# Optimization experiments

Hardware: AMD Instinct MI355X
Metric: run time of the kernel (lower is better)

The kernel has to match this reference:

```python
import jax, jax.numpy as jnp
import numpy as np

N_NODES = 100000
N_EDGES = 625000
D_IN = 128
D_OUT = 128


def setup_inputs() -> dict:
    key = jax.random.key(0)
    k1, k2, k3, k4 = jax.random.split(key, 4)
    embeds = jax.random.normal(k1, (N_NODES, D_IN), dtype=jnp.float32)
    weight = jax.random.normal(k2, (D_IN, D_OUT), dtype=jnp.float32)
    # COO sparse adjacency: row 0 = destination node, row 1 = source node
    edge_index = jax.random.randint(k3, (2, N_DGES := N_EDGES), 0, N_NODES, dtype=jnp.int32)
    edge_vals = jax.random.uniform(k4, (N_EDGES,), dtype=jnp.float32)
    return {"embeds": embeds, "weight": weight, "edge_index": edge_index, "edge_vals": edge_vals}


def reference(embeds, weight, edge_index, edge_vals):
    # support = embeds @ W  -> [N, D_OUT]
    support = jnp.matmul(embeds, weight)
    dst, src = edge_index[0], edge_index[1]
    # spmm: out[d] = sum_{e: dst[e]==d} vals[e] * support[src[e]]
    msgs = edge_vals[:, None] * support[src]  # [E, D_OUT]
    output = jax.ops.segment_sum(msgs, dst, num_segments=embeds.shape[0])
    return output
```

## Files before the change

### kernel.cpp

```cpp
#include <hip/hip_runtime.h>

#define D 128
#define CB 256
#define CB_SHIFT 8
#define NB_MAX 512

typedef __attribute__((ext_vector_type(8))) short short8;
typedef __attribute__((ext_vector_type(4))) float f32x4;

__device__ inline ushort f2bf(float f) {
    uint u = __float_as_uint(f);
    uint r = (u + 0x7FFFu + ((u >> 16) & 1u)) >> 16;
    return (ushort)r;
}

__device__ inline uint cvtpk(float lo, float hi) {
    uint r;
    asm("v_cvt_pk_bf16_f32 %0, %1, %2" : "=v"(r) : "v"(lo), "v"(hi));
    return r;
}


__global__ void zero_f4_kernel(float4* __restrict__ out, int n4) {
    int i = blockIdx.x * blockDim.x + threadIdx.x;
    int stride = gridDim.x * blockDim.x;
    float4 z = make_float4(0.f, 0.f, 0.f, 0.f);
    for (; i < n4; i += stride) out[i] = z;
}


__global__ __launch_bounds__(256) void bucket_hist(const int* __restrict__ dst,
                                                   int* __restrict__ bhist,
                                                   int* __restrict__ cbase,
                                                   int* __restrict__ ccursor, int E,
                                                   const float* __restrict__ W,
                                                   ushort* __restrict__ wT) {
    __shared__ int h[NB_MAX];
    __shared__ int scanbuf[256];
    __shared__ int lastFlag;
    const int t = threadIdx.x;
    #pragma unroll
    for (int j = t; j < NB_MAX; j += 256) h[j] = 0;

    const int gt = blockIdx.x * 256 + t;
    if (gt < D * D) { int r = gt >> 7, c = gt & 127; wT[c * D + r] = f2bf(W[gt]); }
    __syncthreads();

    const int stride = gridDim.x * 256;
    for (int i = gt; i < E; i += stride) atomicAdd(&h[dst[i] >> CB_SHIFT], 1);
    __syncthreads();
    #pragma unroll
    for (int j = t; j < NB_MAX; j += 256)
        if (h[j]) atomicAdd(&bhist[j], h[j]);

    __threadfence();
    __syncthreads();
    if (t == 0) lastFlag = (atomicAdd(&bhist[NB_MAX], 1) == (int)gridDim.x - 1);
    __syncthreads();
    if (!lastFlag) return;

    const int a = atomicAdd(&bhist[2 * t], 0);
    const int b = atomicAdd(&bhist[2 * t + 1], 0);
    const int s = a + b;
    scanbuf[t] = s;
    __syncthreads();
    for (int off = 1; off < 256; off <<= 1) {
        int x = (t >= off) ? scanbuf[t - off] : 0;
        __syncthreads();
        scanbuf[t] += x;
        __syncthreads();
    }
    const int excl = scanbuf[t] - s;
    cbase[2 * t] = excl;         ccursor[2 * t] = excl;
    cbase[2 * t + 1] = excl + a; ccursor[2 * t + 1] = excl + a;
    if (t == 255) cbase[NB_MAX] = excl + s;
}


__global__ __launch_bounds__(512) void gemm_part(const float* __restrict__ embeds,
                                                 const ushort* __restrict__ wT,
                                                 ushort* __restrict__ support, int N,
                                                 const int* __restrict__ dst,
                                                 const int* __restrict__ srcp,
                                                 const float* __restrict__ vals,
                                                 int* __restrict__ ccursor,
                                                 int2* __restrict__ pay1, int E, int npart) {
    __shared__ ushort bLds[D * D];
    __shared__ int phist[NB_MAX];
    __shared__ int pbase[NB_MAX];
    const int t = threadIdx.x;

    if ((int)blockIdx.x < npart) {
        const int ntile = (E + 2047) >> 11;
        for (int tile = blockIdx.x; tile < ntile; tile += npart) {
            const int e0 = tile << 11;
            if (t < NB_MAX) phist[t] = 0;
            __syncthreads();

            int bk[4], rk[4];
            #pragma unroll
            for (int j = 0; j < 4; ++j) {
                int e = e0 + j * 512 + t;
                bk[j] = -1;
                if (e < E) {
                    bk[j] = dst[e] >> CB_SHIFT;
                    rk[j] = atomicAdd(&phist[bk[j]], 1);
                }
            }
            __syncthreads();

            if (t < NB_MAX) pbase[t] = phist[t] ? atomicAdd(&ccursor[t], phist[t]) : 0;
            __syncthreads();

            #pragma unroll
            for (int j = 0; j < 4; ++j) {
                int e = e0 + j * 512 + t;
                if (e >= E) continue;
                int d = dst[e];
                int key = ((d & (CB - 1)) << 17) | srcp[e];
                pay1[pbase[bk[j]] + rk[j]] = make_int2(key, __float_as_int(vals[e]));
            }
            __syncthreads();
        }
        return;
    }

    const int gbid = blockIdx.x - npart;
    const int ngemm = gridDim.x - npart;
    const int w = t >> 6;
    const int l = t & 63;
    const int kgrp = l >> 4;
    const int lan15 = l & 15;

    #pragma unroll
    for (int c = 0; c < 4; ++c) {
        int chunk = c * 512 + t;
        int byteoff = chunk * 16;
        int n = byteoff >> 8;
        int dstoff = byteoff ^ ((n & 7) << 4);
        *(float4*)((char*)bLds + dstoff) = *(const float4*)((const char*)wT + byteoff);
    }
    __syncthreads();

    const int ntiles = (N + 127) >> 7;

    for (int tile = gbid; tile < ntiles; tile += ngemm) {
        const int row0 = tile << 7;
        const int grow = row0 + w * 16 + lan15;
        const bool valid = grow < N;
        const float* arow = embeds + (size_t)grow * D + kgrp * 8;

        float4 pf[8];
        if (valid) {
            #pragma unroll
            for (int ks = 0; ks < 4; ++ks) {
                pf[2 * ks]     = *(const float4*)(arow + ks * 32);
                pf[2 * ks + 1] = *(const float4*)(arow + ks * 32 + 4);
            }
        } else {
            #pragma unroll
            for (int j = 0; j < 8; ++j) pf[j] = make_float4(0.f, 0.f, 0.f, 0.f);
        }

        f32x4 acc[8];
        #pragma unroll
        for (int ct = 0; ct < 8; ++ct) acc[ct] = (f32x4)0.0f;

        #pragma unroll
        for (int ks = 0; ks < 4; ++ks) {
            union { uint4 u; short8 s; } cv;
            const float4 f0 = pf[2 * ks], f1 = pf[2 * ks + 1];
            cv.u.x = cvtpk(f0.x, f0.y);
            cv.u.y = cvtpk(f0.z, f0.w);
            cv.u.z = cvtpk(f1.x, f1.y);
            cv.u.w = cvtpk(f1.z, f1.w);
            const short8 af = cv.s;

            const int kbyte = ks * 64 + kgrp * 16;
            #pragma unroll
            for (int ct = 0; ct < 8; ++ct) {
                const int n = ct * 16 + lan15;
                const int boff = (n * 256 + kbyte) ^ ((n & 7) << 4);
                short8 bfr = *(const short8*)((const char*)bLds + boff);
                acc[ct] = __builtin_amdgcn_mfma_f32_16x16x32_bf16(af, bfr, acc[ct], 0, 0, 0);
            }
        }

        #pragma unroll
        for (int r = 0; r < 4; ++r) {
            const int orow = row0 + w * 16 + kgrp * 4 + r;
            if (orow < N) {
                ushort* srow = &support[(size_t)orow * D + lan15];
                #pragma unroll
                for (int cp = 0; cp < 4; ++cp) {
                    uint u = cvtpk(acc[2 * cp][r], acc[2 * cp + 1][r]);
                    srow[(2 * cp) * 16] = (ushort)u;
                    srow[(2 * cp + 1) * 16] = (ushort)(u >> 16);
                }
            }
        }
    }
}


__global__ __launch_bounds__(256) void finefill2(const int2* __restrict__ pay1,
                                                 const int* __restrict__ cbase,
                                                 int* __restrict__ offsets,
                                                 int2* __restrict__ pay,
                                                 int N, int nb, int E) {
    __shared__ int lcnt[CB];
    __shared__ int bs[CB];
    __shared__ int lofs[CB];
    const int t = threadIdx.x;

    for (int b = blockIdx.x; b < nb; b += gridDim.x) {
        const int beg = cbase[b];
        const int end = cbase[b + 1];
        const int d0 = b << CB_SHIFT;

        lcnt[t] = 0;
        __syncthreads();
        for (int i = beg + t; i < end; i += 256)
            atomicAdd(&lcnt[((unsigned)pay1[i].x) >> 17], 1);
        __syncthreads();

        const int c = lcnt[t];
        bs[t] = c;
        __syncthreads();
        for (int off = 1; off < 256; off <<= 1) {
            int x = (t >= off) ? bs[t - off] : 0;
            __syncthreads();
            bs[t] += x;
            __syncthreads();
        }
        const int run = bs[t] - c + beg;
        if (d0 + t < N) offsets[d0 + t] = run;
        lofs[t] = run;
        __syncthreads();

        for (int i = beg + t; i < end; i += 256) {
            int2 p = pay1[i];
            int dl = ((unsigned)p.x) >> 17;
            int pos = atomicAdd(&lofs[dl], 1);
            pay[pos] = make_int2(p.x & 0x1FFFF, p.y);
        }
        __syncthreads();
    }
    if (blockIdx.x == 0 && t == 0) offsets[N] = E;
}


#define EDGE_MAC(P, M)                                          \
    do {                                                        \
        const float v_ = __int_as_float((P).y);                 \
        acc[0] += v_ * __uint_as_float(((M).x & 0xFFFFu) << 16);\
        acc[1] += v_ * __uint_as_float((M).x & 0xFFFF0000u);    \
        acc[2] += v_ * __uint_as_float(((M).y & 0xFFFFu) << 16);\
        acc[3] += v_ * __uint_as_float((M).y & 0xFFFF0000u);    \
        acc[4] += v_ * __uint_as_float(((M).z & 0xFFFFu) << 16);\
        acc[5] += v_ * __uint_as_float((M).z & 0xFFFF0000u);    \
        acc[6] += v_ * __uint_as_float(((M).w & 0xFFFFu) << 16);\
        acc[7] += v_ * __uint_as_float((M).w & 0xFFFF0000u);    \
    } while (0)

__global__ __launch_bounds__(256, 8) void gather_kernel(const ushort* __restrict__ support,
                                                        const int* __restrict__ offsets,
                                                        const int2* __restrict__ pay,
                                                        float* __restrict__ out, int N) {
    const int gid = (blockIdx.x * 256 + threadIdx.x) >> 4;
    const int sl = threadIdx.x & 15;
    if (gid >= N) return;

    const int beg = offsets[gid];
    const int end = offsets[gid + 1];

    float acc[8];
    #pragma unroll
    for (int j = 0; j < 8; ++j) acc[j] = 0.f;

    int i = beg;
    for (; i + 3 < end; i += 4) {
        const int2 p0 = pay[i], p1 = pay[i + 1], p2 = pay[i + 2], p3 = pay[i + 3];
        const uint4 m0 = *(const uint4*)&support[(size_t)p0.x * D + sl * 8];
        const uint4 m1 = *(const uint4*)&support[(size_t)p1.x * D + sl * 8];
        const uint4 m2 = *(const uint4*)&support[(size_t)p2.x * D + sl * 8];
        const uint4 m3 = *(const uint4*)&support[(size_t)p3.x * D + sl * 8];
        EDGE_MAC(p0, m0); EDGE_MAC(p1, m1); EDGE_MAC(p2, m2); EDGE_MAC(p3, m3);
    }
    for (; i + 1 < end; i += 2) {
        const int2 p0 = pay[i], p1 = pay[i + 1];
        const uint4 m0 = *(const uint4*)&support[(size_t)p0.x * D + sl * 8];
        const uint4 m1 = *(const uint4*)&support[(size_t)p1.x * D + sl * 8];
        EDGE_MAC(p0, m0); EDGE_MAC(p1, m1);
    }
    if (i < end) {
        const int2 p0 = pay[i];
        const uint4 m0 = *(const uint4*)&support[(size_t)p0.x * D + sl * 8];
        EDGE_MAC(p0, m0);
    }

    float* o = &out[(size_t)gid * D + sl * 8];
    *(float4*)o       = make_float4(acc[0], acc[1], acc[2], acc[3]);
    *(float4*)(o + 4) = make_float4(acc[4], acc[5], acc[6], acc[7]);
}


__global__ __launch_bounds__(256) void scatter_kernel(const ushort* __restrict__ support,
                                                      const int* __restrict__ dst,
                                                      const int* __restrict__ src,
                                                      const float* __restrict__ vals,
                                                      float* __restrict__ out, int E) {
    const long long tid = (long long)blockIdx.x * blockDim.x + threadIdx.x;
    const int e = (int)(tid >> 6);
    if (e >= E) return;
    const int c = ((int)tid & 63) * 2;

    const int s = src[e];
    const int d = dst[e];
    const float v = vals[e];

    const uint m = *(const uint*)&support[(size_t)s * D + c];
    const float mx = __uint_as_float((m & 0xFFFFu) << 16);
    const float my = __uint_as_float(m & 0xFFFF0000u);
    atomicAdd(&out[(size_t)d * D + c + 0], v * mx);
    atomicAdd(&out[(size_t)d * D + c + 1], v * my);
}


static inline char* align256(char* p) {
    return (char*)(((uintptr_t)p + 255) & ~(uintptr_t)255);
}

extern "C" void kernel_launch(void* const* d_in, const int* in_sizes, int n_in,
                              void* d_out, int out_size, void* d_ws, size_t ws_size,
                              hipStream_t stream) {
    const float* embeds = (const float*)d_in[0];
    const float* W      = (const float*)d_in[1];
    const int*   eidx   = (const int*)d_in[2];
    const float* vals   = (const float*)d_in[3];

    const int N = in_sizes[0] / D;
    const int E = in_sizes[3];
    const int* dstp = eidx;
    const int* srcp = eidx + E;

    float* out = (float*)d_out;

    char* p = (char*)d_ws;
    ushort* support = (ushort*)p;  p = align256(p + (size_t)N * D * 2);
    ushort* wT      = (ushort*)p;  p = align256(p + (size_t)D * D * 2);
    int* offsets    = (int*)p;     p = align256(p + (size_t)(N + 1) * 4);
    int* bhist      = (int*)p;     p = align256(p + (NB_MAX + 1) * 4);
    int* cbase      = (int*)p;     p = align256(p + (NB_MAX + 1) * 4);
    int* ccursor    = (int*)p;     p = align256(p + NB_MAX * 4);
    int2* pay       = (int2*)p;    p = align256(p + (size_t)E * 8);
    int2* pay1      = (int2*)p;    p = align256(p + (size_t)E * 8);
    const size_t needed = (size_t)(p - (char*)d_ws);

    const int nb = (N + CB - 1) / CB;
    const bool two_level = (N <= (1 << 17)) && (nb <= NB_MAX) && (ws_size >= needed);

    if (two_level) {
        hipMemsetAsync(bhist, 0, (NB_MAX + 1) * 4, stream);
        bucket_hist<<<128, 256, 0, stream>>>(dstp, bhist, cbase, ccursor, E, W, wT);

        const int ntile = (E + 2047) / 2048;
        const int npart = ntile < 512 ? ntile : 512;
        gemm_part<<<npart + 512, 512, 0, stream>>>(embeds, wT, support, N,
                                                   dstp, srcp, vals, ccursor, pay1, E, npart);

        finefill2<<<nb, 256, 0, stream>>>(pay1, cbase, offsets, pay, N, nb, E);
        gather_kernel<<<(N * 16 + 255) / 256, 256, 0, stream>>>(support, offsets, pay, out, N);
    } else {
        hipMemsetAsync(bhist, 0, (NB_MAX + 1) * 4, stream);
        bucket_hist<<<128, 256, 0, stream>>>(dstp, bhist, cbase, ccursor, E, W, wT);
        gemm_part<<<512, 512, 0, stream>>>(embeds, wT, support, N,
                                           dstp, srcp, vals, ccursor, pay1, E, 0);
        zero_f4_kernel<<<2048, 256, 0, stream>>>((float4*)out, out_size / 4);
        const long long nthreads = (long long)E * 64;
        const int blocks = (int)((nthreads + 255) / 256);
        scatter_kernel<<<blocks, 256, 0, stream>>>(support, dstp, srcp, vals, out, E);
    }
}
```

Measured before the change: 92.80 us.

## Split GEMM tiles across partition and fine-fill kernels to overlap work

The dense GEMM now runs in two parts. The first 60% of row tiles are computed alongside the edge partition pass, and the rest run alongside the fine bucket fill in a new fused gemm_fill kernel. The fine fill moves to 512-thread blocks with one bucket per block. The aim is to balance load so the memory-bound fill work overlaps MFMA work instead of running as a separate, underused launch. The bucket_hist grid size is also doubled. This adds a fixed 3/5 split ratio that may not suit other shapes, and gemm_fill blocks carry a large LDS footprint even when they only do fill work.

```diff
diff --git a/kernel.cpp b/kernel.cpp
--- a/kernel.cpp
+++ b/kernel.cpp
@@ -18,6 +18,85 @@
     uint r;
     asm("v_cvt_pk_bf16_f32 %0, %1, %2" : "=v"(r) : "v"(lo), "v"(hi));
     return r;
+}
+
+
+__device__ __forceinline__ void gemm_run(const float* __restrict__ embeds,
+                                         const ushort* __restrict__ wT,
+                                         ushort* __restrict__ support, int N,
+                                         ushort* bLds, int t,
+                                         int tile0, int tileEnd, int stride) {
+    const int w = t >> 6;
+    const int l = t & 63;
+    const int kgrp = l >> 4;
+    const int lan15 = l & 15;
+
+    #pragma unroll
+    for (int c = 0; c < 4; ++c) {
+        int chunk = c * 512 + t;
+        int byteoff = chunk * 16;
+        int n = byteoff >> 8;
+        int dstoff = byteoff ^ ((n & 7) << 4);
+        *(float4*)((char*)bLds + dstoff) = *(const float4*)((const char*)wT + byteoff);
+    }
+    __syncthreads();
+
+    for (int tile = tile0; tile < tileEnd; tile += stride) {
+        const int row0 = tile << 7;
+        const int grow = row0 + w * 16 + lan15;
+        const bool valid = grow < N;
+        const float* arow = embeds + (size_t)grow * D + kgrp * 8;
+
+        float4 pf[8];
+        if (valid) {
+            #pragma unroll
+            for (int ks = 0; ks < 4; ++ks) {
+                pf[2 * ks]     = *(const float4*)(arow + ks * 32);
+                pf[2 * ks + 1] = *(const float4*)(arow + ks * 32 + 4);
+            }
+        } else {
+            #pragma unroll
+            for (int j = 0; j < 8; ++j) pf[j] = make_float4(0.f, 0.f, 0.f, 0.f);
+        }
+
+        f32x4 acc[8];
+        #pragma unroll
+        for (int ct = 0; ct < 8; ++ct) acc[ct] = (f32x4)0.0f;
+
+        #pragma unroll
+        for (int ks = 0; ks < 4; ++ks) {
+            union { uint4 u; short8 s; } cv;
+            const float4 f0 = pf[2 * ks], f1 = pf[2 * ks + 1];
+            cv.u.x = cvtpk(f0.x, f0.y);
+            cv.u.y = cvtpk(f0.z, f0.w);
+            cv.u.z = cvtpk(f1.x, f1.y);
+            cv.u.w = cvtpk(f1.z, f1.w);
+            const short8 af = cv.s;
+
+            const int kbyte = ks * 64 + kgrp * 16;
+            #pragma unroll
+            for (int ct = 0; ct < 8; ++ct) {
+                const int n = ct * 16 + lan15;
+                const int boff = (n * 256 + kbyte) ^ ((n & 7) << 4);
+                short8 bfr = *(const short8*)((const char*)bLds + boff);
+                acc[ct] = __builtin_amdgcn_mfma_f32_16x16x32_bf16(af, bfr, acc[ct], 0, 0, 0);
+            }
+        }
+
+        #pragma unroll
+        for (int r = 0; r < 4; ++r) {
+            const int orow = row0 + w * 16 + kgrp * 4 + r;
+            if (orow < N) {
+                ushort* srow = &support[(size_t)orow * D + lan15];
+                #pragma unroll
+                for (int cp = 0; cp < 4; ++cp) {
+                    uint u = cvtpk(acc[2 * cp][r], acc[2 * cp + 1][r]);
+                    srow[(2 * cp) * 16] = (ushort)u;
+                    srow[(2 * cp + 1) * 16] = (ushort)(u >> 16);
+                }
+            }
+        }
+    }
 }
 
 
@@ -84,7 +163,8 @@
                                                  const int* __restrict__ srcp,
                                                  const float* __restrict__ vals,
                                                  int* __restrict__ ccursor,
-                                                 int2* __restrict__ pay1, int E, int npart) {
+                                                 int2* __restrict__ pay1, int E,
+                                                 int npart, int T1) {
     __shared__ ushort bLds[D * D];
     __shared__ int phist[NB_MAX];
     __shared__ int pbase[NB_MAX];
@@ -125,128 +205,66 @@
         return;
     }
 
-    const int gbid = blockIdx.x - npart;
-    const int ngemm = gridDim.x - npart;
-    const int w = t >> 6;
-    const int l = t & 63;
-    const int kgrp = l >> 4;
-    const int lan15 = l & 15;
-
-    #pragma unroll
-    for (int c = 0; c < 4; ++c) {
-        int chunk = c * 512 + t;
-        int byteoff = chunk * 16;
-        int n = byteoff >> 8;
-        int dstoff = byteoff ^ ((n & 7) << 4);
-        *(float4*)((char*)bLds + dstoff) = *(const float4*)((const char*)wT + byteoff);
-    }
-    __syncthreads();
-
-    const int ntiles = (N + 127) >> 7;
-
-    for (int tile = gbid; tile < ntiles; tile += ngemm) {
-        const int row0 = tile << 7;
-        const int grow = row0 + w * 16 + lan15;
-        const bool valid = grow < N;
-        const float* arow = embeds + (size_t)grow * D + kgrp * 8;
-
-        float4 pf[8];
-        if (valid) {
-            #pragma unroll
-            for (int ks = 0; ks < 4; ++ks) {
-                pf[2 * ks]     = *(const float4*)(arow + ks * 32);
-                pf[2 * ks + 1] = *(const float4*)(arow + ks * 32 + 4);
-            }
-        } else {
-            #pragma unroll
-            for (int j = 0; j < 8; ++j) pf[j] = make_float4(0.f, 0.f, 0.f, 0.f);
-        }
-
-        f32x4 acc[8];
-        #pragma unroll
-        for (int ct = 0; ct < 8; ++ct) acc[ct] = (f32x4)0.0f;
-
-        #pragma unroll
-        for (int ks = 0; ks < 4; ++ks) {
-            union { uint4 u; short8 s; } cv;
-            const float4 f0 = pf[2 * ks], f1 = pf[2 * ks + 1];
-            cv.u.x = cvtpk(f0.x, f0.y);
-            cv.u.y = cvtpk(f0.z, f0.w);
-            cv.u.z = cvtpk(f1.x, f1.y);
-            cv.u.w = cvtpk(f1.z, f1.w);
-            const short8 af = cv.s;
-
-            const int kbyte = ks * 64 + kgrp * 16;
-            #pragma unroll
-            for (int ct = 0; ct < 8; ++ct) {
-                const int n = ct * 16 + lan15;
-                const int boff = (n * 256 + kbyte) ^ ((n & 7) << 4);
-                short8 bfr = *(const short8*)((const char*)bLds + boff);
-                acc[ct] = __builtin_amdgcn_mfma_f32_16x16x32_bf16(af, bfr, acc[ct], 0, 0, 0);
-            }
-        }
-
-        #pragma unroll
-        for (int r = 0; r < 4; ++r) {
-            const int orow = row0 + w * 16 + kgrp * 4 + r;
-            if (orow < N) {
-                ushort* srow = &support[(size_t)orow * D + lan15];
-                #pragma unroll
-                for (int cp = 0; cp < 4; ++cp) {
-                    uint u = cvtpk(acc[2 * cp][r], acc[2 * cp + 1][r]);
-                    srow[(2 * cp) * 16] = (ushort)u;
-                    srow[(2 * cp + 1) * 16] = (ushort)(u >> 16);
-                }
-            }
-        }
-    }
-}
-
-
-__global__ __launch_bounds__(256) void finefill2(const int2* __restrict__ pay1,
+    gemm_run(embeds, wT, support, N, bLds, t,
+             (int)blockIdx.x - npart, T1, (int)gridDim.x - npart);
+}
+
+
+__global__ __launch_bounds__(512) void gemm_fill(const float* __restrict__ embeds,
+                                                 const ushort* __restrict__ wT,
+                                                 ushort* __restrict__ support, int N,
+                                                 const int2* __restrict__ pay1,
                                                  const int* __restrict__ cbase,
                                                  int* __restrict__ offsets,
                                                  int2* __restrict__ pay,
-                                                 int N, int nb, int E) {
+                                                 int nb, int E, int T1) {
+    __shared__ ushort bLds[D * D];
     __shared__ int lcnt[CB];
-    __shared__ int bs[CB];
+    __shared__ int sbuf[512];
     __shared__ int lofs[CB];
     const int t = threadIdx.x;
 
-    for (int b = blockIdx.x; b < nb; b += gridDim.x) {
+    if ((int)blockIdx.x < nb) {
+        const int b = blockIdx.x;
         const int beg = cbase[b];
         const int end = cbase[b + 1];
         const int d0 = b << CB_SHIFT;
 
-        lcnt[t] = 0;
-        __syncthreads();
-        for (int i = beg + t; i < end; i += 256)
+        if (t < CB) lcnt[t] = 0;
+        __syncthreads();
+        for (int i = beg + t; i < end; i += 512)
             atomicAdd(&lcnt[((unsigned)pay1[i].x) >> 17], 1);
         __syncthreads();
 
-        const int c = lcnt[t];
-        bs[t] = c;
-        __syncthreads();
-        for (int off = 1; off < 256; off <<= 1) {
-            int x = (t >= off) ? bs[t - off] : 0;
-            __syncthreads();
-            bs[t] += x;
-            __syncthreads();
-        }
-        const int run = bs[t] - c + beg;
-        if (d0 + t < N) offsets[d0 + t] = run;
-        lofs[t] = run;
-        __syncthreads();
-
-        for (int i = beg + t; i < end; i += 256) {
+        const int c = (t < CB) ? lcnt[t] : 0;
+        sbuf[t] = c;
+        __syncthreads();
+        for (int off = 1; off < 512; off <<= 1) {
+            int x = (t >= off) ? sbuf[t - off] : 0;
+            __syncthreads();
+            sbuf[t] += x;
+            __syncthreads();
+        }
+        if (t < CB) {
+            const int run = sbuf[t] - c + beg;
+            if (d0 + t < N) offsets[d0 + t] = run;
+            lofs[t] = run;
+        }
+        __syncthreads();
+
+        for (int i = beg + t; i < end; i += 512) {
             int2 p = pay1[i];
             int dl = ((unsigned)p.x) >> 17;
             int pos = atomicAdd(&lofs[dl], 1);
             pay[pos] = make_int2(p.x & 0x1FFFF, p.y);
         }
-        __syncthreads();
-    }
-    if (blockIdx.x == 0 && t == 0) offsets[N] = E;
+        if (b == 0 && t == 0) offsets[N] = E;
+        return;
+    }
+
+    const int ntiles = (N + 127) >> 7;
+    gemm_run(embeds, wT, support, N, bLds, t,
+             T1 + (int)blockIdx.x - nb, ntiles, (int)gridDim.x - nb);
 }
 
 
@@ -358,24 +376,29 @@
     const size_t needed = (size_t)(p - (char*)d_ws);
 
     const int nb = (N + CB - 1) / CB;
+    const int ntiles = (N + 127) >> 7;
     const bool two_level = (N <= (1 << 17)) && (nb <= NB_MAX) && (ws_size >= needed);
 
     if (two_level) {
         hipMemsetAsync(bhist, 0, (NB_MAX + 1) * 4, stream);
-        bucket_hist<<<128, 256, 0, stream>>>(dstp, bhist, cbase, ccursor, E, W, wT);
+        bucket_hist<<<256, 256, 0, stream>>>(dstp, bhist, cbase, ccursor, E, W, wT);
 
         const int ntile = (E + 2047) / 2048;
         const int npart = ntile < 512 ? ntile : 512;
+        const int T1 = (ntiles * 3) / 5;
         gemm_part<<<npart + 512, 512, 0, stream>>>(embeds, wT, support, N,
-                                                   dstp, srcp, vals, ccursor, pay1, E, npart);
-
-        finefill2<<<nb, 256, 0, stream>>>(pay1, cbase, offsets, pay, N, nb, E);
+                                                   dstp, srcp, vals, ccursor, pay1, E,
+                                                   npart, T1);
+
+        gemm_fill<<<nb + 512, 512, 0, stream>>>(embeds, wT, support, N,
+                                                pay1, cbase, offsets, pay, nb, E, T1);
+
         gather_kernel<<<(N * 16 + 255) / 256, 256, 0, stream>>>(support, offsets, pay, out, N);
     } else {
         hipMemsetAsync(bhist, 0, (NB_MAX + 1) * 4, stream);
-        bucket_hist<<<128, 256, 0, stream>>>(dstp, bhist, cbase, ccursor, E, W, wT);
+        bucket_hist<<<256, 256, 0, stream>>>(dstp, bhist, cbase, ccursor, E, W, wT);
         gemm_part<<<512, 512, 0, stream>>>(embeds, wT, support, N,
-                                           dstp, srcp, vals, ccursor, pay1, E, 0);
+                                           dstp, srcp, vals, ccursor, pay1, E, 0, ntiles);
         zero_f4_kernel<<<2048, 256, 0, stream>>>((float4*)out, out_size / 4);
         const long long nthreads = (long long)E * 64;
         const int blocks = (int)((nthreads + 255) / 256);
```

New measurement: 97.73 us. 5.3% more time.
